# Optimization experiments

Hardware: AMD Instinct MI355X
Metric: run time of the kernel (lower is better)

## Reference

```python
import jax, jax.numpy as jnp
import numpy as np

CUTOFF = 6.0   # dist_hard_max
BOX = 20.0     # cubic cell edge (Angstrom)
N_IMAGES = 1   # floor(CUTOFF/BOX + eps) + 1 per axis for this cell


def setup_inputs() -> dict:
    key = jax.random.key(0)
    M, N = 8, 400
    coordinates = jax.random.uniform(key, (M, N, 3), dtype=jnp.float32) * BOX
    cell = jnp.tile((BOX * jnp.eye(3, dtype=jnp.float32))[None], (M, 1, 1))
    return {"coordinates": coordinates, "cell": cell}


def reference(coordinates, cell):
    # coordinates: [M, N, 3]; cell: [M, 3, 3]
    M, N, _ = coordinates.shape
    inv_cell = jnp.linalg.inv(cell)                                   # [M,3,3]
    proj = jnp.einsum('mnd,mde->mne', coordinates, inv_cell)          # fractional coords
    wrap_off = jnp.floor(proj)                                        # [M,N,3] wrapped_offset
    wrapped = coordinates - jnp.einsum('mne,med->mnd', wrap_off, cell)  # wrapped coords

    # all image offsets in [-N_IMAGES, N_IMAGES]^3 (27 images)
    rng = jnp.arange(-N_IMAGES, N_IMAGES + 1)
    images = jnp.stack(jnp.meshgrid(rng, rng, rng, indexing='ij'), axis=-1).reshape(-1, 3)  # [K,3]

    shift = jnp.einsum('kc,mcd->mkd', images.astype(cell.dtype), cell)  # [M,K,3]
    drij = wrapped[:, :, None, :] - wrapped[:, None, :, :]              # [M,N,N,3]
    # paircoord[m,k,i,j] = r_i - r_j + image_k @ cell  (identical to torch paircoord values)
    paircoord = drij[:, None] + shift[:, :, None, None, :]             # [M,K,N,N,3]
    d2 = jnp.sum(paircoord * paircoord, axis=-1)                       # [M,K,N,N]

    eye = jnp.eye(N, dtype=bool)
    zero_img = jnp.all(images == 0, axis=-1)                           # [K]
    mask = (d2 < CUTOFF ** 2) & ~(zero_img[None, :, None, None] & eye[None, None, :, :])
    dist = jnp.where(mask, jnp.sqrt(jnp.where(mask, d2, 1.0)), 0.0)    # safe sqrt

    # pair_image = image - (wrap_off_i - wrap_off_j); offset_index as in torch forward
    wo = wrap_off.astype(jnp.int32)
    wij = wo[:, :, None, :] - wo[:, None, :, :]                        # [M,N,N,3]
    pair_image = images.astype(jnp.int32)[None, :, None, None, :] - wij[:, None]  # [M,K,N,N,3]
    n_off = 2 * N_IMAGES + 1
    o = pair_image + N_IMAGES
    offset_index = o[..., 2] + n_off * (o[..., 1] + n_off * o[..., 0])  # [M,K,N,N]

    paircoord_masked = jnp.where(mask[..., None], paircoord, 0.0)
    return dist, paircoord_masked, mask, offset_index
```

## Files before the change

### kernel.cpp

```cpp
#include <hip/hip_runtime.h>

constexpr int M = 8;
constexpr int N = 400;
constexpr int K = 27;
constexpr float CUT2 = 36.0f;
constexpr int D  = M * K * N * N;
constexpr int F4 = D / 4;

typedef float f32x4 __attribute__((ext_vector_type(4)));

constexpr int WS_WRAPPED = 0;
constexpr int WS_WO      = 51200;
constexpr int WS_SHIFT   = 102400;

__global__ __launch_bounds__(128)
void setup_kernel(const float* __restrict__ coords, const float* __restrict__ cell,
                  float4* __restrict__ wrapped, int4* __restrict__ wo,
                  float4* __restrict__ shift)
{
    int m = blockIdx.x;
    const float* c = cell + m * 9;
    float c00 = c[0], c01 = c[1], c02 = c[2];
    float c10 = c[3], c11 = c[4], c12 = c[5];
    float c20 = c[6], c21 = c[7], c22 = c[8];

    float det = c00 * (c11 * c22 - c12 * c21)
              - c01 * (c10 * c22 - c12 * c20)
              + c02 * (c10 * c21 - c11 * c20);
    float rd = 1.0f / det;
    float i00 = (c11 * c22 - c12 * c21) * rd, i01 = (c02 * c21 - c01 * c22) * rd, i02 = (c01 * c12 - c02 * c11) * rd;
    float i10 = (c12 * c20 - c10 * c22) * rd, i11 = (c00 * c22 - c02 * c20) * rd, i12 = (c02 * c10 - c00 * c12) * rd;
    float i20 = (c10 * c21 - c11 * c20) * rd, i21 = (c01 * c20 - c00 * c21) * rd, i22 = (c00 * c11 - c01 * c10) * rd;

    for (int n = threadIdx.x; n < N; n += blockDim.x) {
        int b = (m * N + n) * 3;
        float x = coords[b + 0], y = coords[b + 1], z = coords[b + 2];
        float p0 = x * i00 + y * i10 + z * i20;
        float p1 = x * i01 + y * i11 + z * i21;
        float p2 = x * i02 + y * i12 + z * i22;
        float f0 = floorf(p0), f1 = floorf(p1), f2 = floorf(p2);
        float4 wv;
        wv.x = x - (f0 * c00 + f1 * c10 + f2 * c20);
        wv.y = y - (f0 * c01 + f1 * c11 + f2 * c21);
        wv.z = z - (f0 * c02 + f1 * c12 + f2 * c22);
        wv.w = 0.0f;
        wrapped[m * N + n] = wv;
        int4 ov;
        ov.x = (int)f0; ov.y = (int)f1; ov.z = (int)f2; ov.w = 0;
        wo[m * N + n] = ov;
    }

    if (threadIdx.x < K) {
        int k = threadIdx.x;
        float fx = (float)(k / 9 - 1);
        float fy = (float)((k / 3) % 3 - 1);
        float fz = (float)(k % 3 - 1);
        float4 sv;
        sv.x = fx * c00 + fy * c10 + fz * c20;
        sv.y = fx * c01 + fy * c11 + fz * c21;
        sv.z = fx * c02 + fy * c12 + fz * c22;
        sv.w = 0.0f;
        shift[m * K + k] = sv;
    }
}

__global__ __launch_bounds__(256)
void pairs_kernel(const float4* __restrict__ wrapped, const int4* __restrict__ wo,
                  const float4* __restrict__ shift, float* __restrict__ out)
{
    __shared__ f32x4 lds[3][257];

    int tid = threadIdx.x;
    int t = blockIdx.x * 256 + tid;
    int jq = t % (N / 4);
    int r  = t / (N / 4);
    int i  = r % N;
    int mk = r / N;
    int k  = mk % K;
    int m  = mk / K;
    int j0 = 4 * jq;

    const float4* wrow = wrapped + m * N;
    const int4*   orow = wo      + m * N;

    float4 wj[4];
    int4   oj[4];
    #pragma unroll
    for (int dj = 0; dj < 4; ++dj) { wj[dj] = wrow[j0 + dj]; oj[dj] = orow[j0 + dj]; }
    float4 wi = wrow[i];
    int4   oi = orow[i];
    float4 sh = shift[mk];
    int imx = k / 9 - 1, imy = (k / 3) % 3 - 1, imz = k % 3 - 1;

    float dist[4], msk[4], offv[4], pc[12];
    #pragma unroll
    for (int dj = 0; dj < 4; ++dj) {
        float px = __fadd_rn(__fsub_rn(wi.x, wj[dj].x), sh.x);
        float py = __fadd_rn(__fsub_rn(wi.y, wj[dj].y), sh.y);
        float pz = __fadd_rn(__fsub_rn(wi.z, wj[dj].z), sh.z);
        float d2 = __fadd_rn(__fadd_rn(__fmul_rn(px, px), __fmul_rn(py, py)),
                             __fmul_rn(pz, pz));
        bool mb = (d2 < CUT2) && !((k == (K / 2)) && (i == j0 + dj));
        dist[dj] = mb ? sqrtf(d2) : 0.0f;
        msk[dj]  = mb ? 1.0f : 0.0f;
        pc[3 * dj + 0] = mb ? px : 0.0f;
        pc[3 * dj + 1] = mb ? py : 0.0f;
        pc[3 * dj + 2] = mb ? pz : 0.0f;
        int ox = imx - (oi.x - oj[dj].x) + 1;
        int oy = imy - (oi.y - oj[dj].y) + 1;
        int oz = imz - (oi.z - oj[dj].z) + 1;
        offv[dj] = (float)(oz + 3 * (oy + 3 * ox));
    }

    f32x4 p0 = { pc[0], pc[1], pc[2],  pc[3]  };
    f32x4 p1 = { pc[4], pc[5], pc[6],  pc[7]  };
    f32x4 p2 = { pc[8], pc[9], pc[10], pc[11] };
    lds[0][tid] = p0;
    lds[1][tid] = p1;
    lds[2][tid] = p2;

    f32x4* out4 = reinterpret_cast<f32x4*>(out);
    f32x4 dv = { dist[0], dist[1], dist[2], dist[3] };
    f32x4 mv = { msk[0],  msk[1],  msk[2],  msk[3]  };
    f32x4 ov = { offv[0], offv[1], offv[2], offv[3] };

    out4[t]            = dv;
    out4[4 * F4 + t]   = mv;
    out4[5 * F4 + t]   = ov;

    __builtin_amdgcn_wave_barrier();

    int w64 = tid & ~63;
    int l   = tid & 63;
    int base = F4 + 3 * (blockIdx.x * 256 + w64);
    #pragma unroll
    for (int rr = 0; rr < 3; ++rr) {
        int idx = rr * 64 + l;
        int s2  = idx / 3;
        int q   = idx - 3 * s2;
        out4[base + idx] = lds[q][w64 + s2];
    }
}

extern "C" void kernel_launch(void* const* d_in, const int* in_sizes, int n_in,
                              void* d_out, int out_size, void* d_ws, size_t ws_size,
                              hipStream_t stream) {
    const float* coords = (const float*)d_in[0];
    const float* cell   = (const float*)d_in[1];
    float* out = (float*)d_out;

    char* ws = (char*)d_ws;
    float4* wrapped = (float4*)(ws + WS_WRAPPED);
    int4*   wo      = (int4*)  (ws + WS_WO);
    float4* shift   = (float4*)(ws + WS_SHIFT);

    setup_kernel<<<M, 128, 0, stream>>>(coords, cell, wrapped, wo, shift);

    int total = M * K * N * (N / 4);
    int blocks = total / 256;
    pairs_kernel<<<blocks, 256, 0, stream>>>(wrapped, wo, shift, out);
}
```

Before: 806.5 us.

## Loop nine image shifts per thread, reusing pair differences and index math

Each thread now handles one (i, j-quad) pair for a group of nine consecutive images instead of a single image. The pair differences, offset deltas and the LDS transpose index math are computed once and reused across the nine shifts, and the block size drops to 128. This removes repeated loads and integer work per output, but cuts thread count ninefold and puts nine sets of stores in series per thread, which may reduce memory-level parallelism for a kernel dominated by writes.

```diff
diff --git a/kernel.cpp b/kernel.cpp
--- a/kernel.cpp
+++ b/kernel.cpp
@@ -6,6 +6,9 @@
 constexpr float CUT2 = 36.0f;
 constexpr int D  = M * K * N * N;
 constexpr int F4 = D / 4;
+constexpr int ROW4 = (N * N) / 4;
+constexpr int KG  = 3;
+constexpr int KPT = K / KG;
 
 typedef float f32x4 __attribute__((ext_vector_type(4)));
 
@@ -64,81 +67,103 @@
     }
 }
 
-__global__ __launch_bounds__(256)
+__global__ __launch_bounds__(128)
 void pairs_kernel(const float4* __restrict__ wrapped, const int4* __restrict__ wo,
                   const float4* __restrict__ shift, float* __restrict__ out)
 {
-    __shared__ f32x4 lds[3][257];
+    __shared__ f32x4 lds[3][129];
 
     int tid = threadIdx.x;
-    int t = blockIdx.x * 256 + tid;
-    int jq = t % (N / 4);
-    int r  = t / (N / 4);
-    int i  = r % N;
-    int mk = r / N;
-    int k  = mk % K;
-    int m  = mk / K;
+    int u = blockIdx.x * 128 + tid;
+    int jq = u % 100;
+    int rest = u / 100;
+    int i = rest % 400;
+    int rest2 = rest / 400;
+    int kg = rest2 % 3;
+    int m  = rest2 / 3;
     int j0 = 4 * jq;
 
     const float4* wrow = wrapped + m * N;
     const int4*   orow = wo      + m * N;
 
-    float4 wj[4];
-    int4   oj[4];
+    float4 wj[4]; int4 oj[4];
     #pragma unroll
     for (int dj = 0; dj < 4; ++dj) { wj[dj] = wrow[j0 + dj]; oj[dj] = orow[j0 + dj]; }
     float4 wi = wrow[i];
     int4   oi = orow[i];
-    float4 sh = shift[mk];
-    int imx = k / 9 - 1, imy = (k / 3) % 3 - 1, imz = k % 3 - 1;
 
-    float dist[4], msk[4], offv[4], pc[12];
+    float dx[4], dy[4], dz[4];
+    int offd[4];
+    bool excl[4];
     #pragma unroll
     for (int dj = 0; dj < 4; ++dj) {
-        float px = __fadd_rn(__fsub_rn(wi.x, wj[dj].x), sh.x);
-        float py = __fadd_rn(__fsub_rn(wi.y, wj[dj].y), sh.y);
-        float pz = __fadd_rn(__fsub_rn(wi.z, wj[dj].z), sh.z);
-        float d2 = __fadd_rn(__fadd_rn(__fmul_rn(px, px), __fmul_rn(py, py)),
-                             __fmul_rn(pz, pz));
-        bool mb = (d2 < CUT2) && !((k == (K / 2)) && (i == j0 + dj));
-        dist[dj] = mb ? sqrtf(d2) : 0.0f;
-        msk[dj]  = mb ? 1.0f : 0.0f;
-        pc[3 * dj + 0] = mb ? px : 0.0f;
-        pc[3 * dj + 1] = mb ? py : 0.0f;
-        pc[3 * dj + 2] = mb ? pz : 0.0f;
-        int ox = imx - (oi.x - oj[dj].x) + 1;
-        int oy = imy - (oi.y - oj[dj].y) + 1;
-        int oz = imz - (oi.z - oj[dj].z) + 1;
-        offv[dj] = (float)(oz + 3 * (oy + 3 * ox));
+        dx[dj] = __fsub_rn(wi.x, wj[dj].x);
+        dy[dj] = __fsub_rn(wi.y, wj[dj].y);
+        dz[dj] = __fsub_rn(wi.z, wj[dj].z);
+        offd[dj] = (oi.z - oj[dj].z) + 3 * (oi.y - oj[dj].y) + 9 * (oi.x - oj[dj].x);
+        excl[dj] = (kg == 1) && (i == j0 + dj);
     }
 
-    f32x4 p0 = { pc[0], pc[1], pc[2],  pc[3]  };
-    f32x4 p1 = { pc[4], pc[5], pc[6],  pc[7]  };
-    f32x4 p2 = { pc[8], pc[9], pc[10], pc[11] };
-    lds[0][tid] = p0;
-    lds[1][tid] = p1;
-    lds[2][tid] = p2;
-
-    f32x4* out4 = reinterpret_cast<f32x4*>(out);
-    f32x4 dv = { dist[0], dist[1], dist[2], dist[3] };
-    f32x4 mv = { msk[0],  msk[1],  msk[2],  msk[3]  };
-    f32x4 ov = { offv[0], offv[1], offv[2], offv[3] };
-
-    out4[t]            = dv;
-    out4[4 * F4 + t]   = mv;
-    out4[5 * F4 + t]   = ov;
-
-    __builtin_amdgcn_wave_barrier();
+    int k0 = kg * KPT;
+    int mkbase = m * K + k0;
+    int tbase = (mkbase * N + i) * 100 + jq;
 
     int w64 = tid & ~63;
     int l   = tid & 63;
-    int base = F4 + 3 * (blockIdx.x * 256 + w64);
+    int s2v[3], qv[3];
     #pragma unroll
     for (int rr = 0; rr < 3; ++rr) {
         int idx = rr * 64 + l;
-        int s2  = idx / 3;
-        int q   = idx - 3 * s2;
-        out4[base + idx] = lds[q][w64 + s2];
+        s2v[rr] = idx / 3;
+        qv[rr]  = idx - 3 * s2v[rr];
+    }
+
+    f32x4* out4 = reinterpret_cast<f32x4*>(out);
+
+    #pragma unroll
+    for (int kk = 0; kk < KPT; ++kk) {
+        float4 sh = shift[mkbase + kk];
+        int t = tbase + kk * ROW4;
+        int kcur = k0 + kk;
+
+        float dist[4], msk[4], offv[4], pc[12];
+        #pragma unroll
+        for (int dj = 0; dj < 4; ++dj) {
+            float px = __fadd_rn(dx[dj], sh.x);
+            float py = __fadd_rn(dy[dj], sh.y);
+            float pz = __fadd_rn(dz[dj], sh.z);
+            float d2 = __fadd_rn(__fadd_rn(__fmul_rn(px, px), __fmul_rn(py, py)),
+                                 __fmul_rn(pz, pz));
+            bool mb = (d2 < CUT2);
+            if (kk == 4) mb = mb && !excl[dj];
+            dist[dj] = mb ? sqrtf(d2) : 0.0f;
+            msk[dj]  = mb ? 1.0f : 0.0f;
+            pc[3 * dj + 0] = mb ? px : 0.0f;
+            pc[3 * dj + 1] = mb ? py : 0.0f;
+            pc[3 * dj + 2] = mb ? pz : 0.0f;
+            offv[dj] = (float)(kcur - offd[dj]);
+        }
+
+        f32x4 dv = { dist[0], dist[1], dist[2], dist[3] };
+        f32x4 mv = { msk[0],  msk[1],  msk[2],  msk[3]  };
+        f32x4 ov = { offv[0], offv[1], offv[2], offv[3] };
+        out4[t]          = dv;
+        out4[4 * F4 + t] = mv;
+        out4[5 * F4 + t] = ov;
+
+        f32x4 p0 = { pc[0], pc[1], pc[2],  pc[3]  };
+        f32x4 p1 = { pc[4], pc[5], pc[6],  pc[7]  };
+        f32x4 p2 = { pc[8], pc[9], pc[10], pc[11] };
+        lds[0][tid] = p0;
+        lds[1][tid] = p1;
+        lds[2][tid] = p2;
+        __builtin_amdgcn_wave_barrier();
+        int base = F4 + 3 * (t - l);
+        #pragma unroll
+        for (int rr = 0; rr < 3; ++rr) {
+            out4[base + rr * 64 + l] = lds[qv[rr]][w64 + s2v[rr]];
+        }
+        __builtin_amdgcn_wave_barrier();
     }
 }
 
@@ -156,7 +181,7 @@
 
     setup_kernel<<<M, 128, 0, stream>>>(coords, cell, wrapped, wo, shift);
 
-    int total = M * K * N * (N / 4);
-    int blocks = total / 256;
-    pairs_kernel<<<blocks, 256, 0, stream>>>(wrapped, wo, shift, out);
+    int total = M * KG * N * (N / 4);
+    int blocks = total / 128;
+    pairs_kernel<<<blocks, 128, 0, stream>>>(wrapped, wo, shift, out);
 }
```

Measured after the change: 811.8 us. Within noise of the previous version (+0.7%).
